# Kernel optimization log

Measured on AMD Instinct MI355X. Metric: run time of the kernel, lower is better.

Reference implementation:

```python
import jax, jax.numpy as jnp
import numpy as np

HE_RATIO = 0.005
NP_RATIO = 3.0
THR = 0.01

def setup_inputs() -> dict:
    key = jax.random.key(0)
    k1, k2 = jax.random.split(key)
    B, C, H, W = 32, 2, 768, 768
    x = jax.random.normal(k1, (B, C, H, W), dtype=jnp.float32)
    y = jax.random.uniform(k2, (B, C, H, W), dtype=jnp.float32)
    return {"x": x, "y": y}

def _bce_with_logits(x, y):
    # elementwise BCEWithLogits: softplus(x) - x*y
    return jax.nn.softplus(x) - x * y

def reference(x, y):
    # channel-wise OHEM (chnl_wise=True, keep_pos=False, m=None)
    loss = _bce_with_logits(x, y)                    # [B,C,H,W]
    C, H, W = loss.shape[-3:]
    N = H * W
    loss = loss.reshape(-1, N)                       # [B*C, N]
    pos_mask = (loss < THR).astype(loss.dtype)
    neg_mask = 1.0 - pos_mask
    npos = pos_mask.sum(-1)                          # [R]
    nneg = neg_mask.sum(-1)
    nhe = jnp.where(nneg > NP_RATIO * npos, NP_RATIO * npos, nneg)
    nhe = jnp.maximum(nhe, HE_RATIO * N)
    nhe = jnp.ceil(nhe)                              # per-row keep count
    neg_loss = neg_mask * loss
    # rank of each element in descending order (argsort of argsort),
    # ranking done on detached values as in the original
    key_vals = jax.lax.stop_gradient(neg_loss)
    ranks = jnp.argsort(jnp.argsort(-key_vals, axis=-1), axis=-1)  # [R,N]
    he_mask = (ranks < nhe[:, None]).astype(loss.dtype)
    he_loss = he_mask * neg_loss
    out = (he_loss.sum(-1) / nhe).mean()
    return out
```

## Files before the change

kernel.cpp:

```cpp
#include <hip/hip_runtime.h>

constexpr int R_ = 64;
constexpr int N_ = 768 * 768;
constexpr float THRv = 0.01f;

constexpr float GATE = 1.25f;
constexpr int NB = 1536;
constexpr unsigned int BASE_BITS = 0x3F800000u;
constexpr int SHIFT = 15;
constexpr float FXS = 262144.0f;

constexpr int SUB = 32;
constexpr int F4_PER_BLOCK = (N_ / 4) / SUB;

__global__ __launch_bounds__(256)
void ohem_hist(const float* __restrict__ x, const float* __restrict__ y,
               unsigned long long* __restrict__ hist,
               unsigned int* __restrict__ nnegArr) {
    __shared__ unsigned long long h[NB];
    __shared__ unsigned int sNeg;
    for (int i = threadIdx.x; i < NB; i += 256) h[i] = 0ull;
    if (threadIdx.x == 0) sNeg = 0;
    __syncthreads();

    const int bid = blockIdx.x;
    const int row = (bid & 7) + 8 * ((bid >> 3) & 7);
    const int sub = bid >> 6;

    const size_t base4 = (size_t)row * (N_ / 4) + (size_t)sub * F4_PER_BLOCK;
    const float4* x4 = (const float4*)x;
    const float4* y4 = (const float4*)y;

    int nneg = 0;
    for (int i = threadIdx.x; i < F4_PER_BLOCK; i += 256) {
        float4 xv = x4[base4 + i];
        float4 yv = y4[base4 + i];
        float xs[4] = {xv.x, xv.y, xv.z, xv.w};
        float ys[4] = {yv.x, yv.y, yv.z, yv.w};
#pragma unroll
        for (int j = 0; j < 4; ++j) {
            float e = __expf(-fabsf(xs[j]));
            float l = fmaxf(xs[j], 0.0f) - xs[j] * ys[j] + __logf(1.0f + e);
            nneg += (l >= THRv);
            if (l >= GATE) {
                unsigned int idx = (__float_as_uint(l) - BASE_BITS) >> SHIFT;
                if (idx > NB - 1) idx = NB - 1;
                atomicAdd(&h[idx],
                          (1ull << 43) + (unsigned long long)(l * FXS + 0.5f));
            }
        }
    }
    if (nneg) atomicAdd(&sNeg, (unsigned int)nneg);
    __syncthreads();

    unsigned long long* rh = hist + (size_t)row * NB;
    for (int i = threadIdx.x; i < NB; i += 256)
        if (h[i]) atomicAdd(&rh[i], h[i]);
    if (threadIdx.x == 0) atomicAdd(&nnegArr[row], sNeg);
}

__global__ __launch_bounds__(256)
void ohem_select(const unsigned long long* __restrict__ hist,
                 const unsigned int* __restrict__ nnegArr,
                 float* __restrict__ out) {
    __shared__ unsigned int cnt[NB];
    __shared__ float sums[NB];
    __shared__ unsigned int segCnt[256];
    __shared__ float segSum[256];
    const int row = blockIdx.x;
    const int tid = threadIdx.x;

    unsigned int c0 = 0;
    float s0 = 0.0f;
    for (int i = tid * 6; i < tid * 6 + 6; ++i) {
        unsigned long long p = hist[(size_t)row * NB + i];
        unsigned int c = (unsigned int)(p >> 43);
        float s = (float)(p & ((1ull << 43) - 1)) * (1.0f / FXS);
        cnt[i] = c;
        sums[i] = s;
        c0 += c;
        s0 += s;
    }
    segCnt[tid] = c0;
    segSum[tid] = s0;
    __syncthreads();

    if (tid == 0) {
        const float nnegf = (float)nnegArr[row];
        const float nposf = (float)N_ - nnegf;
        float nhe = fminf(nnegf, 3.0f * nposf);
        nhe = fmaxf(nhe, 0.005f * (float)N_);
        nhe = ceilf(nhe);
        const long long k = (long long)nhe;

        long long cum = 0;
        float sumAb = 0.0f;
        int seg = 255;
        for (; seg >= 0; --seg) {
            if (cum + (long long)segCnt[seg] >= k) break;
            cum += segCnt[seg];
            sumAb += segSum[seg];
        }
        float res;
        if (seg < 0) {
            res = sumAb / nhe;
        } else {
            int bstar = seg * 6;
            for (int i = seg * 6 + 5; i >= seg * 6; --i) {
                if (cum + (long long)cnt[i] >= k) { bstar = i; break; }
                cum += cnt[i];
                sumAb += sums[i];
            }
            const float rem = (float)(k - cum);
            const float c = (float)cnt[bstar];
            const float lo = __uint_as_float(BASE_BITS + ((unsigned)bstar << SHIFT));
            const float w = lo * (1.0f / 256.0f);
            const float mean = sums[bstar] / c;
            const float topAvg = mean + (1.0f - rem / c) * 0.5f * w;
            res = (sumAb + rem * topAvg) / nhe;
        }
        atomicAdd(out, res * (1.0f / (float)R_));
    }
}

extern "C" void kernel_launch(void* const* d_in, const int* in_sizes, int n_in,
                              void* d_out, int out_size, void* d_ws, size_t ws_size,
                              hipStream_t stream) {
    const float* x = (const float*)d_in[0];
    const float* y = (const float*)d_in[1];
    float* out = (float*)d_out;

    unsigned long long* hist = (unsigned long long*)d_ws;
    unsigned int* nnegArr = (unsigned int*)(hist + (size_t)R_ * NB);

    hipMemsetAsync(d_ws, 0,
                   (size_t)R_ * NB * sizeof(unsigned long long) +
                       R_ * sizeof(unsigned int),
                   stream);
    hipMemsetAsync(d_out, 0, sizeof(float), stream);

    ohem_hist<<<R_ * SUB, 256, 0, stream>>>(x, y, hist, nnegArr);
    ohem_select<<<R_, 256, 0, stream>>>(hist, nnegArr, out);
}
```

Baseline: 78.62 us.

## Fuse histogram and selection kernels via last-block ticket, unroll loads, cheaper softplus

Merges the select kernel into the histogram kernel: each row's last-finishing block, found through an atomic ticket counter, reads the global histogram and computes that row's result. The main loop now issues three float4 loads of x and y up front per iteration to raise memory-level parallelism. Softplus is rewritten as log(1+exp(x)) using hardware exp2/log builtins. This removes one kernel launch and its tail, at the cost of a threadfence plus atomic reads in every block. The unguarded exp can overflow to inf for large x, which would change the loss for those elements.

```diff
diff --git a/kernel.cpp b/kernel.cpp
--- a/kernel.cpp
+++ b/kernel.cpp
@@ -2,7 +2,7 @@
 
 constexpr int R_ = 64;
 constexpr int N_ = 768 * 768;
-constexpr float THRv = 0.01f;
+constexpr float THRc = 0.01f;
 
 constexpr float GATE = 1.25f;
 constexpr int NB = 1536;
@@ -13,12 +13,20 @@
 constexpr int SUB = 32;
 constexpr int F4_PER_BLOCK = (N_ / 4) / SUB;
 
+constexpr float LOG2E = 1.4426950408889634f;
+constexpr float LN2 = 0.6931471805599453f;
+
 __global__ __launch_bounds__(256)
-void ohem_hist(const float* __restrict__ x, const float* __restrict__ y,
-               unsigned long long* __restrict__ hist,
-               unsigned int* __restrict__ nnegArr) {
+void ohem_fused(const float* __restrict__ x, const float* __restrict__ y,
+                unsigned long long* __restrict__ hist,
+                unsigned int* __restrict__ nnegArr,
+                unsigned int* __restrict__ ticket,
+                float* __restrict__ out) {
     __shared__ unsigned long long h[NB];
     __shared__ unsigned int sNeg;
+    __shared__ unsigned int sTicket;
+    __shared__ unsigned int segCnt[256];
+    __shared__ float segSum[256];
     for (int i = threadIdx.x; i < NB; i += 256) h[i] = 0ull;
     if (threadIdx.x == 0) sNeg = 0;
     __syncthreads();
@@ -32,21 +40,29 @@
     const float4* y4 = (const float4*)y;
 
     int nneg = 0;
-    for (int i = threadIdx.x; i < F4_PER_BLOCK; i += 256) {
-        float4 xv = x4[base4 + i];
-        float4 yv = y4[base4 + i];
-        float xs[4] = {xv.x, xv.y, xv.z, xv.w};
-        float ys[4] = {yv.x, yv.y, yv.z, yv.w};
+    for (int it = 0; it < 6; ++it) {
+        const int i = it * 768 + threadIdx.x;
+        float4 xv[3], yv[3];
 #pragma unroll
-        for (int j = 0; j < 4; ++j) {
-            float e = __expf(-fabsf(xs[j]));
-            float l = fmaxf(xs[j], 0.0f) - xs[j] * ys[j] + __logf(1.0f + e);
-            nneg += (l >= THRv);
-            if (l >= GATE) {
-                unsigned int idx = (__float_as_uint(l) - BASE_BITS) >> SHIFT;
-                if (idx > NB - 1) idx = NB - 1;
-                atomicAdd(&h[idx],
-                          (1ull << 43) + (unsigned long long)(l * FXS + 0.5f));
+        for (int u = 0; u < 3; ++u) xv[u] = x4[base4 + i + u * 256];
+#pragma unroll
+        for (int u = 0; u < 3; ++u) yv[u] = y4[base4 + i + u * 256];
+#pragma unroll
+        for (int u = 0; u < 3; ++u) {
+            float xs[4] = {xv[u].x, xv[u].y, xv[u].z, xv[u].w};
+            float ys[4] = {yv[u].x, yv[u].y, yv[u].z, yv[u].w};
+#pragma unroll
+            for (int j = 0; j < 4; ++j) {
+                float a = __builtin_amdgcn_exp2f(xs[j] * LOG2E);
+                float l = fmaf(__builtin_amdgcn_logf(1.0f + a), LN2,
+                               -xs[j] * ys[j]);
+                nneg += (l >= THRc);
+                if (l >= GATE) {
+                    unsigned int idx = (__float_as_uint(l) - BASE_BITS) >> SHIFT;
+                    if (idx > NB - 1) idx = NB - 1;
+                    atomicAdd(&h[idx],
+                              (1ull << 43) + (unsigned long long)(l * FXS + 0.5f));
+                }
             }
         }
     }
@@ -57,23 +73,21 @@
     for (int i = threadIdx.x; i < NB; i += 256)
         if (h[i]) atomicAdd(&rh[i], h[i]);
     if (threadIdx.x == 0) atomicAdd(&nnegArr[row], sNeg);
-}
 
-__global__ __launch_bounds__(256)
-void ohem_select(const unsigned long long* __restrict__ hist,
-                 const unsigned int* __restrict__ nnegArr,
-                 float* __restrict__ out) {
-    __shared__ unsigned int cnt[NB];
-    __shared__ float sums[NB];
-    __shared__ unsigned int segCnt[256];
-    __shared__ float segSum[256];
-    const int row = blockIdx.x;
+    __threadfence();
+    if (threadIdx.x == 0) sTicket = atomicAdd(&ticket[row], 1u);
+    __syncthreads();
+    if (sTicket != SUB - 1) return;
+
+    unsigned int* cnt = (unsigned int*)h;
+    float* sums = (float*)(cnt + NB);
     const int tid = threadIdx.x;
-
     unsigned int c0 = 0;
     float s0 = 0.0f;
-    for (int i = tid * 6; i < tid * 6 + 6; ++i) {
-        unsigned long long p = hist[(size_t)row * NB + i];
+#pragma unroll
+    for (int b = 0; b < 6; ++b) {
+        const int i = tid * 6 + b;
+        unsigned long long p = atomicAdd(&rh[i], 0ull);
         unsigned int c = (unsigned int)(p >> 43);
         float s = (float)(p & ((1ull << 43) - 1)) * (1.0f / FXS);
         cnt[i] = c;
@@ -86,7 +100,7 @@
     __syncthreads();
 
     if (tid == 0) {
-        const float nnegf = (float)nnegArr[row];
+        const float nnegf = (float)atomicAdd(&nnegArr[row], 0u);
         const float nposf = (float)N_ - nnegf;
         float nhe = fminf(nnegf, 3.0f * nposf);
         nhe = fmaxf(nhe, 0.005f * (float)N_);
@@ -132,13 +146,12 @@
 
     unsigned long long* hist = (unsigned long long*)d_ws;
     unsigned int* nnegArr = (unsigned int*)(hist + (size_t)R_ * NB);
+    unsigned int* ticket = nnegArr + R_;
 
-    hipMemsetAsync(d_ws, 0,
-                   (size_t)R_ * NB * sizeof(unsigned long long) +
-                       R_ * sizeof(unsigned int),
-                   stream);
+    const size_t zeroBytes = (size_t)R_ * NB * sizeof(unsigned long long) +
+                             2 * R_ * sizeof(unsigned int);
+    hipMemsetAsync(d_ws, 0, zeroBytes, stream);
     hipMemsetAsync(d_out, 0, sizeof(float), stream);
 
-    ohem_hist<<<R_ * SUB, 256, 0, stream>>>(x, y, hist, nnegArr);
-    ohem_select<<<R_, 256, 0, stream>>>(hist, nnegArr, out);
+    ohem_fused<<<R_ * SUB, 256, 0, stream>>>(x, y, hist, nnegArr, ticket, out);
 }
```

Result: slower. 277.2 us (+252.5%).
